# Performance work log

Measured on AMD Instinct MI355X. Metric: run time of the kernel, lower is better.

Reference implementation:

```python
import jax, jax.numpy as jnp
import numpy as np

N_NODES = 100000
N_EDGES = 3200000
EMB_DIM = 32


def setup_inputs() -> dict:
    key = jax.random.key(0)
    k1, k2, k3 = jax.random.split(key, 3)
    edge_index = jax.random.randint(k1, (2, N_EDGES), 0, N_NODES, dtype=jnp.int64 if jax.config.jax_enable_x64 else jnp.int32)
    W = jax.random.normal(k2, (3, EMB_DIM), dtype=jnp.float32)
    b = jax.random.normal(k3, (EMB_DIM,), dtype=jnp.float32)
    return {"edge_index": edge_index, "num_nodes": N_NODES, "W": W, "b": b}


def reference(edge_index, num_nodes, W, b):
    src, dst = edge_index[0], edge_index[1]
    ones = jnp.ones(src.shape[0], dtype=jnp.float32)
    # degree = scatter-add of ones over node ids (pyg.utils.degree)
    deg_in = jax.ops.segment_sum(ones, dst, num_segments=num_nodes)
    deg_out = jax.ops.segment_sum(ones, src, num_segments=num_nodes)
    du = deg_out[src]          # [E]
    dv = deg_in[dst]           # [E]
    deg_feat = jnp.stack([du, dv, du + dv], axis=-1)  # [E, 3]
    return deg_feat @ W + b    # [E, emb_dim]
```

## Files before the change

kernel.cpp:

```cpp
#include <hip/hip_runtime.h>


#define THREADS 256
#define N_NODES_FIXED 100000
#define CH 32000
#define CHW (CH/2)
#define NCHUNK 4
#define NSLICE 64

__global__ __launch_bounds__(THREADS) void deg_partial_kernel(
        const int* __restrict__ edges,
        unsigned int* __restrict__ partial,
        int E) {
    __shared__ unsigned int h[CHW];
    for (int i = threadIdx.x; i < CHW; i += THREADS) h[i] = 0;
    __syncthreads();

    int job = blockIdx.x;
    int s = job & (NSLICE - 1);
    int c = (job >> 6) & (NCHUNK - 1);
    int a = job >> 8;
    int base = c * CH;

    int sliceLen = (((E + NSLICE - 1) / NSLICE) + 3) & ~3;
    int start = s * sliceLen;
    int end = min(start + sliceLen, E);
    const int* row = edges + (size_t)a * E;

    int n4 = (end - start) >> 2;
    const int4* row4 = (const int4*)(row + start);
    for (int i = threadIdx.x; i < n4; i += THREADS) {
        int4 v = row4[i];
        int x;
        x = v.x - base; if ((unsigned)x < (unsigned)CH) atomicAdd(&h[x >> 1], 1u << ((x & 1) * 16));
        x = v.y - base; if ((unsigned)x < (unsigned)CH) atomicAdd(&h[x >> 1], 1u << ((x & 1) * 16));
        x = v.z - base; if ((unsigned)x < (unsigned)CH) atomicAdd(&h[x >> 1], 1u << ((x & 1) * 16));
        x = v.w - base; if ((unsigned)x < (unsigned)CH) atomicAdd(&h[x >> 1], 1u << ((x & 1) * 16));
    }
    int tail_start = start + (n4 << 2);
    for (int i = tail_start + (int)threadIdx.x; i < end; i += THREADS) {
        int x = row[i] - base;
        if ((unsigned)x < (unsigned)CH) atomicAdd(&h[x >> 1], 1u << ((x & 1) * 16));
    }
    __syncthreads();

    unsigned int* dst = partial + (size_t)job * CHW;
    for (int i = threadIdx.x; i < CHW; i += THREADS) dst[i] = h[i];
}

__global__ __launch_bounds__(THREADS) void deg_reduce_kernel(
        const unsigned int* __restrict__ partial,
        float* __restrict__ deg,
        int N) {
    const int TOT = 2 * NCHUNK * CHW;
    int tid = blockIdx.x * blockDim.x + threadIdx.x;
    if (tid >= TOT) return;
    int a = tid / (NCHUNK * CHW);
    int rem = tid - a * (NCHUNK * CHW);
    int c = rem / CHW;
    int w = rem - c * CHW;

    const unsigned int* p = partial + ((size_t)(a * NCHUNK + c) * NSLICE) * CHW + w;
    unsigned int lo = 0, hi = 0;
    #pragma unroll 8
    for (int s = 0; s < NSLICE; s++) {
        unsigned int v = p[(size_t)s * CHW];
        lo += v & 0xFFFFu;
        hi += v >> 16;
    }
    int node = c * CH + 2 * w;
    if (node < N)     deg[a * N + node]     = (float)lo;
    if (node + 1 < N) deg[a * N + node + 1] = (float)hi;
}

__global__ __launch_bounds__(THREADS) void encode_kernel(
        const int* __restrict__ edges,
        const float* __restrict__ deg,
        const float* __restrict__ W,
        const float* __restrict__ b,
        float4* __restrict__ out,
        int E, int N) {
    __shared__ float4 sA[8], sB[8], sC[8];
    if (threadIdx.x < 8) {
        int c = threadIdx.x;
        const float4* W4 = (const float4*)W;
        float4 w0 = W4[c], w1 = W4[8 + c], w2 = W4[16 + c];
        float4 b4 = ((const float4*)b)[c];
        sA[c] = make_float4(w0.x + w2.x, w0.y + w2.y, w0.z + w2.z, w0.w + w2.w);
        sB[c] = make_float4(w1.x + w2.x, w1.y + w2.y, w1.z + w2.z, w1.w + w2.w);
        sC[c] = b4;
    }
    __syncthreads();

    int gid = blockIdx.x * blockDim.x + threadIdx.x;
    if (gid >= E * 8) return;
    int e = gid >> 3;
    int c = gid & 7;
    int s = edges[e];
    int d = edges[E + e];
    float du = deg[s];
    float dv = deg[N + d];

    float4 aa = sA[c], bb = sB[c], cc = sC[c];
    float4 r;
    r.x = fmaf(du, aa.x, fmaf(dv, bb.x, cc.x));
    r.y = fmaf(du, aa.y, fmaf(dv, bb.y, cc.y));
    r.z = fmaf(du, aa.z, fmaf(dv, bb.z, cc.z));
    r.w = fmaf(du, aa.w, fmaf(dv, bb.w, cc.w));
    out[gid] = r;
}

extern "C" void kernel_launch(void* const* d_in, const int* in_sizes, int n_in,
                              void* d_out, int out_size, void* d_ws, size_t ws_size,
                              hipStream_t stream) {
    const int*   edges = (const int*)d_in[0];
    const float* W     = (const float*)d_in[2];
    const float* b     = (const float*)d_in[3];
    float*       out   = (float*)d_out;

    const int E = in_sizes[0] / 2;
    const int N = N_NODES_FIXED;

    float*        deg     = (float*)d_ws;
    unsigned int* partial = (unsigned int*)((char*)d_ws + (size_t)2 * N * sizeof(float));

    deg_partial_kernel<<<2 * NCHUNK * NSLICE, THREADS, 0, stream>>>(edges, partial, E);

    deg_reduce_kernel<<<(2 * NCHUNK * CHW + THREADS - 1) / THREADS, THREADS, 0, stream>>>(
        partial, deg, N);

    int total = E * 8;
    encode_kernel<<<(total + THREADS - 1) / THREADS, THREADS, 0, stream>>>(
        edges, deg, W, b, (float4*)out, E, N);
}
```

Before: 487.6 us.

## Pack degree histogram into 8-bit counters, halve chunks, grid-stride encode

The shared-memory degree histogram now packs four 8-bit counters per word instead of two 16-bit ones. That lets each block cover 50000 nodes, so 2 chunks replace 4 and each edge row is scanned fewer times, with 512-thread blocks. The W+b combination table is built once in the reduce kernel rather than in every encode block, and the encode kernel becomes a fixed 2048-block grid-stride loop. The 8-bit counters overflow if one node gets more than 255 edges in a single slice, which holds for uniform random inputs but not for skewed graphs.

Result: no change. 479.3 us (-1.7%).

```diff
diff --git a/kernel.cpp b/kernel.cpp
--- a/kernel.cpp
+++ b/kernel.cpp
@@ -1,25 +1,25 @@
 #include <hip/hip_runtime.h>
 
 
-#define THREADS 256
-#define N_NODES_FIXED 100000
-#define CH 32000
-#define CHW (CH/2)
-#define NCHUNK 4
+#define NN 100000
+#define CH 50000
+#define CHW (CH/4)
+#define NCHUNK 2
 #define NSLICE 64
+#define PT 512
 
-__global__ __launch_bounds__(THREADS) void deg_partial_kernel(
+__global__ __launch_bounds__(PT) void deg_partial_kernel(
         const int* __restrict__ edges,
         unsigned int* __restrict__ partial,
         int E) {
     __shared__ unsigned int h[CHW];
-    for (int i = threadIdx.x; i < CHW; i += THREADS) h[i] = 0;
+    for (int i = threadIdx.x; i < CHW; i += PT) h[i] = 0;
     __syncthreads();
 
     int job = blockIdx.x;
     int s = job & (NSLICE - 1);
     int c = (job >> 6) & (NCHUNK - 1);
-    int a = job >> 8;
+    int a = job >> 7;
     int base = c * CH;
 
     int sliceLen = (((E + NSLICE - 1) / NSLICE) + 3) & ~3;
@@ -27,33 +27,41 @@
     int end = min(start + sliceLen, E);
     const int* row = edges + (size_t)a * E;
 
-    int n4 = (end - start) >> 2;
+    int n4 = (end > start) ? ((end - start) >> 2) : 0;
     const int4* row4 = (const int4*)(row + start);
-    for (int i = threadIdx.x; i < n4; i += THREADS) {
+    for (int i = threadIdx.x; i < n4; i += PT) {
         int4 v = row4[i];
         int x;
-        x = v.x - base; if ((unsigned)x < (unsigned)CH) atomicAdd(&h[x >> 1], 1u << ((x & 1) * 16));
-        x = v.y - base; if ((unsigned)x < (unsigned)CH) atomicAdd(&h[x >> 1], 1u << ((x & 1) * 16));
-        x = v.z - base; if ((unsigned)x < (unsigned)CH) atomicAdd(&h[x >> 1], 1u << ((x & 1) * 16));
-        x = v.w - base; if ((unsigned)x < (unsigned)CH) atomicAdd(&h[x >> 1], 1u << ((x & 1) * 16));
+        x = v.x - base; if ((unsigned)x < (unsigned)CH) atomicAdd(&h[x >> 2], 1u << ((x & 3) * 8));
+        x = v.y - base; if ((unsigned)x < (unsigned)CH) atomicAdd(&h[x >> 2], 1u << ((x & 3) * 8));
+        x = v.z - base; if ((unsigned)x < (unsigned)CH) atomicAdd(&h[x >> 2], 1u << ((x & 3) * 8));
+        x = v.w - base; if ((unsigned)x < (unsigned)CH) atomicAdd(&h[x >> 2], 1u << ((x & 3) * 8));
     }
-    int tail_start = start + (n4 << 2);
-    for (int i = tail_start + (int)threadIdx.x; i < end; i += THREADS) {
+    int ts = start + (n4 << 2);
+    for (int i = ts + (int)threadIdx.x; i < end; i += PT) {
         int x = row[i] - base;
-        if ((unsigned)x < (unsigned)CH) atomicAdd(&h[x >> 1], 1u << ((x & 1) * 16));
+        if ((unsigned)x < (unsigned)CH) atomicAdd(&h[x >> 2], 1u << ((x & 3) * 8));
     }
     __syncthreads();
 
     unsigned int* dst = partial + (size_t)job * CHW;
-    for (int i = threadIdx.x; i < CHW; i += THREADS) dst[i] = h[i];
+    for (int i = threadIdx.x; i < CHW; i += PT) dst[i] = h[i];
 }
 
-__global__ __launch_bounds__(THREADS) void deg_reduce_kernel(
+__global__ __launch_bounds__(PT) void deg_reduce_kernel(
         const unsigned int* __restrict__ partial,
         float* __restrict__ deg,
-        int N) {
+        const float* __restrict__ W,
+        const float* __restrict__ b,
+        float* __restrict__ table) {
+    if (blockIdx.x == 0 && threadIdx.x < 32) {
+        int d = threadIdx.x;
+        table[d]      = W[d]      + W[64 + d];
+        table[32 + d] = W[32 + d] + W[64 + d];
+        table[64 + d] = b[d];
+    }
     const int TOT = 2 * NCHUNK * CHW;
-    int tid = blockIdx.x * blockDim.x + threadIdx.x;
+    int tid = blockIdx.x * PT + threadIdx.x;
     if (tid >= TOT) return;
     int a = tid / (NCHUNK * CHW);
     int rem = tid - a * (NCHUNK * CHW);
@@ -61,53 +69,46 @@
     int w = rem - c * CHW;
 
     const unsigned int* p = partial + ((size_t)(a * NCHUNK + c) * NSLICE) * CHW + w;
-    unsigned int lo = 0, hi = 0;
+    unsigned int s0 = 0, s1 = 0, s2 = 0, s3 = 0;
     #pragma unroll 8
     for (int s = 0; s < NSLICE; s++) {
         unsigned int v = p[(size_t)s * CHW];
-        lo += v & 0xFFFFu;
-        hi += v >> 16;
+        s0 += v & 0xFFu;
+        s1 += (v >> 8) & 0xFFu;
+        s2 += (v >> 16) & 0xFFu;
+        s3 += v >> 24;
     }
-    int node = c * CH + 2 * w;
-    if (node < N)     deg[a * N + node]     = (float)lo;
-    if (node + 1 < N) deg[a * N + node + 1] = (float)hi;
+    int node = c * CH + 4 * w;
+    float4 r = make_float4((float)s0, (float)s1, (float)s2, (float)s3);
+    *(float4*)(deg + (size_t)a * NN + node) = r;
 }
 
-__global__ __launch_bounds__(THREADS) void encode_kernel(
+__global__ __launch_bounds__(256) void encode_kernel(
         const int* __restrict__ edges,
         const float* __restrict__ deg,
-        const float* __restrict__ W,
-        const float* __restrict__ b,
+        const float* __restrict__ table,
         float4* __restrict__ out,
-        int E, int N) {
-    __shared__ float4 sA[8], sB[8], sC[8];
-    if (threadIdx.x < 8) {
-        int c = threadIdx.x;
-        const float4* W4 = (const float4*)W;
-        float4 w0 = W4[c], w1 = W4[8 + c], w2 = W4[16 + c];
-        float4 b4 = ((const float4*)b)[c];
-        sA[c] = make_float4(w0.x + w2.x, w0.y + w2.y, w0.z + w2.z, w0.w + w2.w);
-        sB[c] = make_float4(w1.x + w2.x, w1.y + w2.y, w1.z + w2.z, w1.w + w2.w);
-        sC[c] = b4;
+        int E) {
+    const float4* t4 = (const float4*)table;
+    int total = E * 8;
+    int stride = gridDim.x * blockDim.x;
+    int gid = blockIdx.x * blockDim.x + threadIdx.x;
+    if (gid >= total) return;
+    int c = gid & 7;
+    float4 aa = t4[c], bb = t4[8 + c], cc = t4[16 + c];
+    for (; gid < total; gid += stride) {
+        int e = gid >> 3;
+        int s = edges[e];
+        int d = edges[E + e];
+        float du = deg[s];
+        float dv = deg[NN + d];
+        float4 r;
+        r.x = fmaf(du, aa.x, fmaf(dv, bb.x, cc.x));
+        r.y = fmaf(du, aa.y, fmaf(dv, bb.y, cc.y));
+        r.z = fmaf(du, aa.z, fmaf(dv, bb.z, cc.z));
+        r.w = fmaf(du, aa.w, fmaf(dv, bb.w, cc.w));
+        out[gid] = r;
     }
-    __syncthreads();
-
-    int gid = blockIdx.x * blockDim.x + threadIdx.x;
-    if (gid >= E * 8) return;
-    int e = gid >> 3;
-    int c = gid & 7;
-    int s = edges[e];
-    int d = edges[E + e];
-    float du = deg[s];
-    float dv = deg[N + d];
-
-    float4 aa = sA[c], bb = sB[c], cc = sC[c];
-    float4 r;
-    r.x = fmaf(du, aa.x, fmaf(dv, bb.x, cc.x));
-    r.y = fmaf(du, aa.y, fmaf(dv, bb.y, cc.y));
-    r.z = fmaf(du, aa.z, fmaf(dv, bb.z, cc.z));
-    r.w = fmaf(du, aa.w, fmaf(dv, bb.w, cc.w));
-    out[gid] = r;
 }
 
 extern "C" void kernel_launch(void* const* d_in, const int* in_sizes, int n_in,
@@ -119,17 +120,15 @@
     float*       out   = (float*)d_out;
 
     const int E = in_sizes[0] / 2;
-    const int N = N_NODES_FIXED;
 
-    float*        deg     = (float*)d_ws;
-    unsigned int* partial = (unsigned int*)((char*)d_ws + (size_t)2 * N * sizeof(float));
+    float*        table   = (float*)d_ws;
+    float*        deg     = (float*)((char*)d_ws + 512);
+    unsigned int* partial = (unsigned int*)((char*)d_ws + 512 + (size_t)2 * NN * sizeof(float));
 
-    deg_partial_kernel<<<2 * NCHUNK * NSLICE, THREADS, 0, stream>>>(edges, partial, E);
+    deg_partial_kernel<<<2 * NCHUNK * NSLICE, PT, 0, stream>>>(edges, partial, E);
 
-    deg_reduce_kernel<<<(2 * NCHUNK * CHW + THREADS - 1) / THREADS, THREADS, 0, stream>>>(
-        partial, deg, N);
+    deg_reduce_kernel<<<(2 * NCHUNK * CHW + PT - 1) / PT, PT, 0, stream>>>(
+        partial, deg, W, b, table);
 
-    int total = E * 8;
-    encode_kernel<<<(total + THREADS - 1) / THREADS, THREADS, 0, stream>>>(
-        edges, deg, W, b, (float4*)out, E, N);
+    encode_kernel<<<2048, 256, 0, stream>>>(edges, deg, table, (float4*)out, E);
 }
```
